# Performance work log

Hardware: AMD Instinct MI355X
Metric: run time of the kernel (lower is better)

The kernel has to match this reference:

```python
import jax, jax.numpy as jnp
import numpy as np

N = 100000   # nodes
E = 1600000  # edges
F_IN = 64
HID = 64
N_HLIN = 64
N_PRED = 1
G = 128      # graphs in batch


def setup_inputs() -> dict:
    key = jax.random.key(0)
    ks = jax.random.split(key, 12)
    x = jax.random.normal(ks[0], (N, F_IN), dtype=jnp.float32)
    edge_index = jax.random.randint(ks[1], (2, E), 0, N, dtype=jnp.int64)
    batch = jnp.sort(jax.random.randint(ks[2], (N,), 0, G, dtype=jnp.int64))
    def glorot(k, fan_in, fan_out):
        return jax.random.normal(k, (fan_in, fan_out), dtype=jnp.float32) / np.float32(np.sqrt(fan_in))
    return {
        "x": x, "edge_index": edge_index, "batch": batch,
        "W1": glorot(ks[3], F_IN, HID), "b1": jnp.zeros((HID,), jnp.float32),
        "W2": glorot(ks[4], HID, HID),  "b2": jnp.zeros((HID,), jnp.float32),
        "W3": glorot(ks[5], HID, HID),  "b3": jnp.zeros((HID,), jnp.float32),
        "W4": glorot(ks[6], HID, N_HLIN), "b4": jnp.zeros((N_HLIN,), jnp.float32),
        "lin_w": glorot(ks[7], N_HLIN, N_PRED),
        "lin_b": jnp.zeros((N_PRED,), jnp.float32),
    }


def reference(x, edge_index, batch, W1, b1, W2, b2, W3, b3, W4, b4, lin_w, lin_b):
    # GCNConv semantics (PyG default): add self-loops, symmetric deg^-1/2 normalization,
    # h' = scatter_add(norm * (h W)[src] -> dst) + b
    loop = jnp.arange(N, dtype=edge_index.dtype)
    src = jnp.concatenate([edge_index[0], loop])  # [E+N]
    dst = jnp.concatenate([edge_index[1], loop])  # [E+N]
    deg = jax.ops.segment_sum(jnp.ones_like(dst, dtype=x.dtype), dst, num_segments=N)
    dis = deg ** -0.5  # deg >= 1 thanks to self-loops
    norm = (dis[src] * dis[dst])[:, None]  # [E+N, 1]

    def gcn_conv(h, W, b):
        h = h @ W                      # [N, out]
        msg = h[src] * norm            # edge gather + scale
        agg = jax.ops.segment_sum(msg, dst, num_segments=N)  # scatter-add
        return agg + b

    h = jax.nn.relu(gcn_conv(x, W1, b1))
    h = jax.nn.relu(gcn_conv(h, W2, b2))
    h = jax.nn.relu(gcn_conv(h, W3, b3))
    h = gcn_conv(h, W4, b4)

    # global_mean_pool over graph ids
    sums = jax.ops.segment_sum(h, batch, num_segments=G)          # [G, N_HLIN]
    cnts = jax.ops.segment_sum(jnp.ones((N,), h.dtype), batch, num_segments=G)
    pooled = sums / jnp.maximum(cnts, 1.0)[:, None]
    # dropout is identity in eval mode
    return pooled @ lin_w + lin_b  # [G, N_PRED]
```

## Files before the change

### kernel.cpp

```cpp
#include <hip/hip_runtime.h>
#include <type_traits>

#define NN 100000
#define NE 1600000
#define FD 64
#define NG 128
#define NB ((NN + 255) >> 8)
#define CAP 6144
#define SRCMASK 0x1FFFF
#define ZR NN
#define NPAD 100032

typedef _Float16 f16x8 __attribute__((ext_vector_type(8)));
typedef float f32x4 __attribute__((ext_vector_type(4)));

__global__ void bhist_k(const int* __restrict__ dst, int* __restrict__ bhist) {
    __shared__ int h[NB];
    int t = threadIdx.x;
    for (int i = t; i < NB; i += 256) h[i] = 0;
    __syncthreads();
    int base = blockIdx.x * 4096;
#pragma unroll
    for (int i = 0; i < 16; i++) {
        int e = base + i * 256 + t;
        if (e < NE) atomicAdd(&h[dst[e] >> 8], 1);
    }
    __syncthreads();
    for (int i = t; i < NB; i += 256)
        if (h[i]) atomicAdd(&bhist[i], h[i]);
}

__global__ void bscan_k(const int* __restrict__ bhist, int* __restrict__ bbase,
                        int* __restrict__ gcursor, _Float16* __restrict__ zrowA,
                        _Float16* __restrict__ zrowB) {
    __shared__ int sS[512];
    int t = threadIdx.x;
    if (t < 8)  ((int4*)zrowA)[t] = make_int4(0, 0, 0, 0);
    if (t >= 8 && t < 16) ((int4*)zrowB)[t - 8] = make_int4(0, 0, 0, 0);
    sS[t] = (t < NB) ? bhist[t] : 0;
    __syncthreads();
    for (int off = 1; off < 512; off <<= 1) {
        int x = (t >= off) ? sS[t - off] : 0;
        __syncthreads();
        if (t >= off) sS[t] += x;
        __syncthreads();
    }
    int excl = (t == 0) ? 0 : sS[t - 1];
    if (t < NB) { bbase[t] = excl; gcursor[t] = excl; }
    if (t == NB) bbase[NB] = NE;
}

__global__ void part1_k(const int* __restrict__ src, const int* __restrict__ dst,
                        int* __restrict__ gcursor, int* __restrict__ part) {
    __shared__ int hist[NB];
    __shared__ int resv[NB];
    __shared__ int lcur[NB];
    int t = threadIdx.x;
    for (int i = t; i < NB; i += 256) { hist[i] = 0; lcur[i] = 0; }
    __syncthreads();
    int base = blockIdx.x * 4096;
    int s[16], d[16];
#pragma unroll
    for (int i = 0; i < 16; i++) {
        int e = base + i * 256 + t;
        if (e < NE) {
            s[i] = src[e]; d[i] = dst[e];
            atomicAdd(&hist[d[i] >> 8], 1);
        } else d[i] = -1;
    }
    __syncthreads();
    for (int b = t; b < NB; b += 256)
        if (hist[b]) resv[b] = atomicAdd(&gcursor[b], hist[b]);
    __syncthreads();
#pragma unroll
    for (int i = 0; i < 16; i++) {
        if (d[i] >= 0) {
            int b = d[i] >> 8;
            int off = atomicAdd(&lcur[b], 1);
            part[resv[b] + off] = s[i] | ((d[i] & 255) << 17);
        }
    }
}

__global__ void csr2_k(const int* __restrict__ part, const int* __restrict__ bbase,
                       int* __restrict__ rowptr, float* __restrict__ dis,
                       int* __restrict__ entries, int* __restrict__ dbins) {
    __shared__ int sA[CAP];
    __shared__ int sB[CAP];
    __shared__ int cntL[256];
    __shared__ int posL[256];
    __shared__ int locL[256];
    __shared__ int dbL[64];
    int b = blockIdx.x, t = threadIdx.x;
    int n0 = b << 8;
    int nCnt = min(256, NN - n0);
    cntL[t] = 0; posL[t] = 0;
    if (t < 64) dbL[t] = 0;
    __syncthreads();
    int e0 = bbase[b], e1 = bbase[b + 1];
    int cnt = e1 - e0;

    for (int i = t; i < cnt; i += 256) {
        int pk = part[e0 + i];
        if (i < CAP) sA[i] = pk;
        atomicAdd(&cntL[(pk >> 17) & 255], 1);
    }
    __syncthreads();

    if (t < nCnt) atomicAdd(&dbL[min(cntL[t], 63)], 1);

    locL[t] = cntL[t];
    __syncthreads();
    for (int off = 1; off < 256; off <<= 1) {
        int x = (t >= off) ? locL[t - off] : 0;
        __syncthreads();
        if (t >= off) locL[t] += x;
        __syncthreads();
    }
    int excl = (t == 0) ? 0 : locL[t - 1];
    __syncthreads();
    locL[t] = excl;
    __syncthreads();

    if (t < nCnt) {
        rowptr[n0 + t] = e0 + locL[t];
        dis[n0 + t] = rsqrtf((float)cntL[t] + 1.0f);
    }
    if (b == NB - 1 && t == 0) rowptr[NN] = NE;
    if (t < 64 && dbL[t]) atomicAdd(&dbins[t], dbL[t]);

    for (int i = t; i < cnt; i += 256) {
        int pk = (i < CAP) ? sA[i] : part[e0 + i];
        int ln = (pk >> 17) & 255;
        int sv = pk & SRCMASK;
        int pos = atomicAdd(&posL[ln], 1);
        int idx = locL[ln] + pos;
        if (idx < CAP) sB[idx] = sv;
        else entries[e0 + idx] = sv;
    }
    __syncthreads();
    int lim = min(cnt, CAP);
    for (int i = t; i < lim; i += 256)
        entries[e0 + i] = sB[i];
}

__global__ void dscan_k(const int* __restrict__ dbins, int* __restrict__ dcursor,
                        int* __restrict__ perm) {
    int t = threadIdx.x;
    int orig = dbins[t];
    int v = orig;
    for (int off = 1; off < 64; off <<= 1) {
        int x = __shfl_up(v, off);
        if (t >= off) v += x;
    }
    dcursor[t] = v - orig;
    if (t < NPAD - NN) perm[NN + t] = -1;
}

__global__ void dfill_k(const int* __restrict__ rowptr, int* __restrict__ dcursor,
                        int* __restrict__ perm) {
    __shared__ int h[64], resv[64], lpos[64];
    int t = threadIdx.x;
    int n = blockIdx.x * 256 + t;
    if (t < 64) { h[t] = 0; lpos[t] = 0; }
    __syncthreads();
    int bin = -1;
    if (n < NN) {
        int deg = rowptr[n + 1] - rowptr[n];
        bin = min(deg, 63);
        atomicAdd(&h[bin], 1);
    }
    __syncthreads();
    if (t < 64 && h[t]) resv[t] = atomicAdd(&dcursor[t], h[t]);
    __syncthreads();
    if (n < NN) {
        int pos = atomicAdd(&lpos[bin], 1);
        perm[resv[bin] + pos] = n;
    }
}

template <typename TIN>
__global__ __launch_bounds__(256) void gemm_mfma_k(const TIN* __restrict__ h,
                                                   const float* __restrict__ W,
                                                   const float* __restrict__ dis,
                                                   _Float16* __restrict__ out16) {
    __shared__ _Float16 wT[64 * 76];
    __shared__ _Float16 oS[64 * 64];
    int t = threadIdx.x;
    int wave = t >> 6, lane = t & 63;
    int m0 = blockIdx.x * 64 + wave * 16;
    int arow = min(m0 + (lane & 15), NN - 1);
    int kg = lane >> 4;

    f16x8 a0, a1;
    if constexpr (std::is_same<TIN, float>::value) {
        const float4* p0 = (const float4*)&h[(size_t)arow * 64 + kg * 8];
        const float4* p1 = (const float4*)&h[(size_t)arow * 64 + 32 + kg * 8];
        float4 x0 = p0[0], x1 = p0[1], y0 = p1[0], y1 = p1[1];
        a0[0] = (_Float16)x0.x; a0[1] = (_Float16)x0.y; a0[2] = (_Float16)x0.z; a0[3] = (_Float16)x0.w;
        a0[4] = (_Float16)x1.x; a0[5] = (_Float16)x1.y; a0[6] = (_Float16)x1.z; a0[7] = (_Float16)x1.w;
        a1[0] = (_Float16)y0.x; a1[1] = (_Float16)y0.y; a1[2] = (_Float16)y0.z; a1[3] = (_Float16)y0.w;
        a1[4] = (_Float16)y1.x; a1[5] = (_Float16)y1.y; a1[6] = (_Float16)y1.z; a1[7] = (_Float16)y1.w;
    } else {
        a0 = *(const f16x8*)&h[(size_t)arow * 64 + kg * 8];
        a1 = *(const f16x8*)&h[(size_t)arow * 64 + 32 + kg * 8];
    }

    for (int i = t; i < 4096; i += 256) {
        int k = i >> 6, c = i & 63;
        wT[c * 76 + k] = (_Float16)W[i];
    }
    __syncthreads();

    f32x4 acc[4];
#pragma unroll
    for (int i = 0; i < 4; i++) acc[i] = (f32x4){0.f, 0.f, 0.f, 0.f};

#pragma unroll
    for (int c0 = 0; c0 < 4; c0++) {
        const _Float16* wp = &wT[(c0 * 16 + (lane & 15)) * 76 + kg * 8];
        f16x8 b0 = *(const f16x8*)wp;
        f16x8 b1 = *(const f16x8*)(wp + 32);
        acc[c0] = __builtin_amdgcn_mfma_f32_16x16x32_f16(a0, b0, acc[c0], 0, 0, 0);
        acc[c0] = __builtin_amdgcn_mfma_f32_16x16x32_f16(a1, b1, acc[c0], 0, 0, 0);
    }

#pragma unroll
    for (int j = 0; j < 4; j++) {
        int row = (lane >> 4) * 4 + j;
        float dsc = dis[min(m0 + row, NN - 1)];
#pragma unroll
        for (int c0 = 0; c0 < 4; c0++)
            oS[(wave * 16 + row) * 64 + c0 * 16 + (lane & 15)] = (_Float16)(acc[c0][j] * dsc);
    }
    __syncthreads();

    int rbase = blockIdx.x * 64;
    for (int i = t; i < 512; i += 256) {
        int r = i >> 3;
        if (rbase + r < NN)
            ((int4*)&out16[(size_t)(rbase + r) * 64])[i & 7] = ((int4*)oS)[i];
    }
}

template <int LAST>
__global__ void gather_k(const _Float16* __restrict__ h2p, const int* __restrict__ rowptr,
                         const int* __restrict__ entries, const float* __restrict__ dis,
                         const float* __restrict__ bias, const int* __restrict__ perm,
                         _Float16* __restrict__ out16, float* __restrict__ outf) {
    int wave = (blockIdx.x * blockDim.x + threadIdx.x) >> 6;
    int lane = threadIdx.x & 63;
    int g = lane >> 3;
    int k = lane & 7;
    int fo = k * 8;
    int gb = g << 3;

    int n = perm[wave * 8 + g];
    bool valid = n >= 0;
    int nc = valid ? n : 0;
    int e0 = rowptr[nc];
    int cnt = valid ? (rowptr[nc + 1] - e0 + 1) : 0;

    int m = cnt;
    m = max(m, __shfl_xor(m, 8));
    m = max(m, __shfl_xor(m, 16));
    m = max(m, __shfl_xor(m, 32));
    int nch = (m + 7) >> 3;

    float ac[8];
#pragma unroll
    for (int i = 0; i < 8; i++) ac[i] = 0.f;

    int entA = (k == 0) ? (valid ? n : ZR)
             : ((k < cnt) ? entries[e0 + k - 1] : ZR);

    for (int ch = 0; ch < nch; ++ch) {
        int itk2 = ((ch + 1) << 3) + k;
        int entB = (itk2 < cnt) ? entries[e0 + itk2 - 1] : ZR;
#pragma unroll
        for (int c = 0; c < 8; ++c) {
            int s = __shfl(entA, gb | c);
            f16x8 v = *(const f16x8*)&h2p[(size_t)s * 64 + fo];
#pragma unroll
            for (int i = 0; i < 8; ++i) ac[i] += (float)v[i];
        }
        entA = entB;
    }

    if (valid) {
        float dn = dis[n];
        float4 b0 = *(const float4*)&bias[fo];
        float4 b1 = *(const float4*)&bias[fo + 4];
        float r0 = b0.x + dn * ac[0], r1 = b0.y + dn * ac[1];
        float r2 = b0.z + dn * ac[2], r3 = b0.w + dn * ac[3];
        float r4 = b1.x + dn * ac[4], r5 = b1.y + dn * ac[5];
        float r6 = b1.z + dn * ac[6], r7 = b1.w + dn * ac[7];
        if (LAST) {
            *(float4*)&outf[(size_t)n * 64 + fo]     = make_float4(r0, r1, r2, r3);
            *(float4*)&outf[(size_t)n * 64 + fo + 4] = make_float4(r4, r5, r6, r7);
        } else {
            f16x8 o;
            o[0] = (_Float16)fmaxf(r0, 0.f); o[1] = (_Float16)fmaxf(r1, 0.f);
            o[2] = (_Float16)fmaxf(r2, 0.f); o[3] = (_Float16)fmaxf(r3, 0.f);
            o[4] = (_Float16)fmaxf(r4, 0.f); o[5] = (_Float16)fmaxf(r5, 0.f);
            o[6] = (_Float16)fmaxf(r6, 0.f); o[7] = (_Float16)fmaxf(r7, 0.f);
            *(f16x8*)&out16[(size_t)n * 64 + fo] = o;
        }
    }
}

__global__ void pool_acc_k(const float* __restrict__ h, const int* __restrict__ batch,
                           float* __restrict__ pool) {
    int wid = (blockIdx.x * blockDim.x + threadIdx.x) >> 6;
    int lane = threadIdx.x & 63;
    int n0 = wid * 32;
    if (n0 >= NN) return;
    int n1 = min(n0 + 32, NN);
    int g = batch[n0];
    float acc = 0.0f;
    for (int n = n0; n < n1; n++) {
        int gn = batch[n];
        if (gn != g) {
            atomicAdd(&pool[g * FD + lane], acc);
            acc = 0.0f;
            g = gn;
        }
        acc += h[(size_t)n * FD + lane];
    }
    atomicAdd(&pool[g * FD + lane], acc);
}

__global__ void cnt_k(const int* __restrict__ batch, float* __restrict__ cnt,
                      float* __restrict__ pool) {
    int t = threadIdx.x;
    for (int i = t; i < NG * FD; i += 128) pool[i] = 0.f;
    if (t >= NG) return;
    auto lb = [&](int key) {
        int lo = 0, hi = NN;
        while (lo < hi) {
            int mid = (lo + hi) >> 1;
            if (batch[mid] < key) lo = mid + 1; else hi = mid;
        }
        return lo;
    };
    cnt[t] = (float)(lb(t + 1) - lb(t));
}

__global__ void final_k(const float* __restrict__ pool, const float* __restrict__ cnt,
                        const float* __restrict__ lin_w, const float* __restrict__ lin_b,
                        float* __restrict__ out) {
    int g = blockIdx.x * blockDim.x + threadIdx.x;
    if (g >= NG) return;
    float c = fmaxf(cnt[g], 1.0f);
    float s = 0.0f;
    for (int f = 0; f < FD; f++) s += pool[g * FD + f] * lin_w[f];
    out[g] = s / c + lin_b[0];
}

extern "C" void kernel_launch(void* const* d_in, const int* in_sizes, int n_in,
                              void* d_out, int out_size, void* d_ws, size_t ws_size,
                              hipStream_t stream) {
    const float* x     = (const float*)d_in[0];
    const int*   src   = (const int*)d_in[1];
    const int*   dst   = ((const int*)d_in[1]) + NE;
    const int*   batch = (const int*)d_in[2];
    const float* W1 = (const float*)d_in[3];  const float* b1 = (const float*)d_in[4];
    const float* W2 = (const float*)d_in[5];  const float* b2 = (const float*)d_in[6];
    const float* W3 = (const float*)d_in[7];  const float* b3 = (const float*)d_in[8];
    const float* W4 = (const float*)d_in[9];  const float* b4 = (const float*)d_in[10];
    const float* lin_w = (const float*)d_in[11];
    const float* lin_b = (const float*)d_in[12];
    float* out = (float*)d_out;

    char* p = (char*)d_ws;
    float*    aggf    = (float*)p;
    int*      part    = (int*)p;      p += (size_t)NN * FD * 4;
    _Float16* h16a    = (_Float16*)p; p += (size_t)(NN + 1) * FD * 2;
    _Float16* h16b    = (_Float16*)p; p += (size_t)(NN + 1) * FD * 2;
    int*      entries = (int*)p;      p += (size_t)NE * 4;
    float*    dis     = (float*)p;    p += (size_t)NN * 4;
    int*      rowptr  = (int*)p;      p += (size_t)(NN + 4) * 4;
    int*      bhist   = (int*)p;      p += ((NB + 3) & ~3) * 4;
    int*      dbins   = (int*)p;      p += 64 * 4;
    int*      bbase   = (int*)p;      p += ((NB + 4) & ~3) * 4;
    int*      gcursor = (int*)p;      p += ((NB + 3) & ~3) * 4;
    int*      dcursor = (int*)p;      p += 64 * 4;
    int*      perm    = (int*)p;      p += (size_t)NPAD * 4;
    float*    pool    = (float*)p;    p += (size_t)NG * FD * 4;
    float*    cnt     = (float*)p;    p += (size_t)NG * 4;

    const int EGRID = (NE + 4095) / 4096;

    hipMemsetAsync(bhist, 0, (((NB + 3) & ~3) + 64) * 4, stream);
    bhist_k<<<EGRID, 256, 0, stream>>>(dst, bhist);
    bscan_k<<<1, 512, 0, stream>>>(bhist, bbase, gcursor,
                                   h16a + (size_t)ZR * FD, h16b + (size_t)ZR * FD);
    part1_k<<<EGRID, 256, 0, stream>>>(src, dst, gcursor, part);
    csr2_k<<<NB, 256, 0, stream>>>(part, bbase, rowptr, dis, entries, dbins);
    dscan_k<<<1, 64, 0, stream>>>(dbins, dcursor, perm);
    dfill_k<<<NB, 256, 0, stream>>>(rowptr, dcursor, perm);

    const int GEMM_GRID = (NN + 63) / 64;
    const int GATHER_GRID = NPAD / 32;

    gemm_mfma_k<float><<<GEMM_GRID, 256, 0, stream>>>(x, W1, dis, h16b);
    gather_k<0><<<GATHER_GRID, 256, 0, stream>>>(h16b, rowptr, entries, dis, b1, perm, h16a, nullptr);
    gemm_mfma_k<_Float16><<<GEMM_GRID, 256, 0, stream>>>(h16a, W2, dis, h16b);
    gather_k<0><<<GATHER_GRID, 256, 0, stream>>>(h16b, rowptr, entries, dis, b2, perm, h16a, nullptr);
    gemm_mfma_k<_Float16><<<GEMM_GRID, 256, 0, stream>>>(h16a, W3, dis, h16b);
    gather_k<0><<<GATHER_GRID, 256, 0, stream>>>(h16b, rowptr, entries, dis, b3, perm, h16a, nullptr);
    gemm_mfma_k<_Float16><<<GEMM_GRID, 256, 0, stream>>>(h16a, W4, dis, h16b);
    gather_k<1><<<GATHER_GRID, 256, 0, stream>>>(h16b, rowptr, entries, dis, b4, perm, nullptr, aggf);

    cnt_k<<<1, 128, 0, stream>>>(batch, cnt, pool);
    pool_acc_k<<<((NN + 31) / 32 * 64 + 255) / 256, 256, 0, stream>>>(aggf, batch, pool);
    final_k<<<1, 128, 0, stream>>>(pool, cnt, lin_w, lin_b, out);
}
```

Baseline: 290.2 us.

## Replace global degree-sort permutation with per-block local degree bucketing in csr2

Drops the global degree-binned permutation, which needed a dbins reduction, a dscan kernel and a dfill kernel. Each csr2 block now sorts its own 256 nodes by degree bin into its slice of perm, using a shared histogram and a wave scan. The perm padding init moves into bscan. This removes two kernel launches and a pass over rowptr, but degree grouping now holds only within 256-node windows, which may give the gather kernels less even load balance.

```diff
diff --git a/kernel.cpp b/kernel.cpp
--- a/kernel.cpp
+++ b/kernel.cpp
@@ -32,11 +32,12 @@
 
 __global__ void bscan_k(const int* __restrict__ bhist, int* __restrict__ bbase,
                         int* __restrict__ gcursor, _Float16* __restrict__ zrowA,
-                        _Float16* __restrict__ zrowB) {
+                        _Float16* __restrict__ zrowB, int* __restrict__ perm) {
     __shared__ int sS[512];
     int t = threadIdx.x;
     if (t < 8)  ((int4*)zrowA)[t] = make_int4(0, 0, 0, 0);
     if (t >= 8 && t < 16) ((int4*)zrowB)[t - 8] = make_int4(0, 0, 0, 0);
+    if (t < NPAD - NN) perm[NN + t] = -1;
     sS[t] = (t < NB) ? bhist[t] : 0;
     __syncthreads();
     for (int off = 1; off < 512; off <<= 1) {
@@ -84,18 +85,18 @@
 
 __global__ void csr2_k(const int* __restrict__ part, const int* __restrict__ bbase,
                        int* __restrict__ rowptr, float* __restrict__ dis,
-                       int* __restrict__ entries, int* __restrict__ dbins) {
+                       int* __restrict__ entries, int* __restrict__ perm) {
     __shared__ int sA[CAP];
     __shared__ int sB[CAP];
     __shared__ int cntL[256];
     __shared__ int posL[256];
     __shared__ int locL[256];
-    __shared__ int dbL[64];
+    __shared__ int hb[64], hcur[64];
     int b = blockIdx.x, t = threadIdx.x;
     int n0 = b << 8;
     int nCnt = min(256, NN - n0);
     cntL[t] = 0; posL[t] = 0;
-    if (t < 64) dbL[t] = 0;
+    if (t < 64) { hb[t] = 0; }
     __syncthreads();
     int e0 = bbase[b], e1 = bbase[b + 1];
     int cnt = e1 - e0;
@@ -107,10 +108,22 @@
     }
     __syncthreads();
 
-    if (t < nCnt) atomicAdd(&dbL[min(cntL[t], 63)], 1);
+    int bin = -1;
+    if (t < nCnt) { bin = min(cntL[t], 63); atomicAdd(&hb[bin], 1); }
 
     locL[t] = cntL[t];
     __syncthreads();
+
+    if (t < 64) {
+        int orig = hb[t];
+        int v = orig;
+        for (int off = 1; off < 64; off <<= 1) {
+            int x = __shfl_up(v, off);
+            if (t >= off) v += x;
+        }
+        hcur[t] = v - orig;
+    }
+
     for (int off = 1; off < 256; off <<= 1) {
         int x = (t >= off) ? locL[t - off] : 0;
         __syncthreads();
@@ -125,9 +138,10 @@
     if (t < nCnt) {
         rowptr[n0 + t] = e0 + locL[t];
         dis[n0 + t] = rsqrtf((float)cntL[t] + 1.0f);
+        int pos = atomicAdd(&hcur[bin], 1);
+        perm[n0 + pos] = n0 + t;
     }
     if (b == NB - 1 && t == 0) rowptr[NN] = NE;
-    if (t < 64 && dbL[t]) atomicAdd(&dbins[t], dbL[t]);
 
     for (int i = t; i < cnt; i += 256) {
         int pk = (i < CAP) ? sA[i] : part[e0 + i];
@@ -142,41 +156,6 @@
     int lim = min(cnt, CAP);
     for (int i = t; i < lim; i += 256)
         entries[e0 + i] = sB[i];
-}
-
-__global__ void dscan_k(const int* __restrict__ dbins, int* __restrict__ dcursor,
-                        int* __restrict__ perm) {
-    int t = threadIdx.x;
-    int orig = dbins[t];
-    int v = orig;
-    for (int off = 1; off < 64; off <<= 1) {
-        int x = __shfl_up(v, off);
-        if (t >= off) v += x;
-    }
-    dcursor[t] = v - orig;
-    if (t < NPAD - NN) perm[NN + t] = -1;
-}
-
-__global__ void dfill_k(const int* __restrict__ rowptr, int* __restrict__ dcursor,
-                        int* __restrict__ perm) {
-    __shared__ int h[64], resv[64], lpos[64];
-    int t = threadIdx.x;
-    int n = blockIdx.x * 256 + t;
-    if (t < 64) { h[t] = 0; lpos[t] = 0; }
-    __syncthreads();
-    int bin = -1;
-    if (n < NN) {
-        int deg = rowptr[n + 1] - rowptr[n];
-        bin = min(deg, 63);
-        atomicAdd(&h[bin], 1);
-    }
-    __syncthreads();
-    if (t < 64 && h[t]) resv[t] = atomicAdd(&dcursor[t], h[t]);
-    __syncthreads();
-    if (n < NN) {
-        int pos = atomicAdd(&lpos[bin], 1);
-        perm[resv[bin] + pos] = n;
-    }
 }
 
 template <typename TIN>
@@ -381,24 +360,20 @@
     float*    dis     = (float*)p;    p += (size_t)NN * 4;
     int*      rowptr  = (int*)p;      p += (size_t)(NN + 4) * 4;
     int*      bhist   = (int*)p;      p += ((NB + 3) & ~3) * 4;
-    int*      dbins   = (int*)p;      p += 64 * 4;
     int*      bbase   = (int*)p;      p += ((NB + 4) & ~3) * 4;
     int*      gcursor = (int*)p;      p += ((NB + 3) & ~3) * 4;
-    int*      dcursor = (int*)p;      p += 64 * 4;
     int*      perm    = (int*)p;      p += (size_t)NPAD * 4;
     float*    pool    = (float*)p;    p += (size_t)NG * FD * 4;
     float*    cnt     = (float*)p;    p += (size_t)NG * 4;
 
     const int EGRID = (NE + 4095) / 4096;
 
-    hipMemsetAsync(bhist, 0, (((NB + 3) & ~3) + 64) * 4, stream);
+    hipMemsetAsync(bhist, 0, ((NB + 3) & ~3) * 4, stream);
     bhist_k<<<EGRID, 256, 0, stream>>>(dst, bhist);
     bscan_k<<<1, 512, 0, stream>>>(bhist, bbase, gcursor,
-                                   h16a + (size_t)ZR * FD, h16b + (size_t)ZR * FD);
+                                   h16a + (size_t)ZR * FD, h16b + (size_t)ZR * FD, perm);
     part1_k<<<EGRID, 256, 0, stream>>>(src, dst, gcursor, part);
-    csr2_k<<<NB, 256, 0, stream>>>(part, bbase, rowptr, dis, entries, dbins);
-    dscan_k<<<1, 64, 0, stream>>>(dbins, dcursor, perm);
-    dfill_k<<<NB, 256, 0, stream>>>(rowptr, dcursor, perm);
+    csr2_k<<<NB, 256, 0, stream>>>(part, bbase, rowptr, dis, entries, perm);
 
     const int GEMM_GRID = (NN + 63) / 64;
     const int GATHER_GRID = NPAD / 32;
```

After: 301.9 us. +4.0%, slower.
